# Optimization experiments

Measured on AMD Instinct MI355X. Metric: run time of the kernel, lower is better.

Reference implementation:

```python
import jax, jax.numpy as jnp
import numpy as np

H = 16        # head_nums
DN = 128      # qk_nope_head_dim
DR = 64       # qk_rope_head_dim
DV = 128      # v_head_dim
QLR = 1536    # q_lora_rank
KVLR = 512    # kv_lora_rank
HID = 2048    # hidden_dim
THETA = 10000.0
EPS = 1e-6


def _rms(x, w):
    return x * jax.lax.rsqrt(jnp.mean(x * x, axis=-1, keepdims=True) + EPS) * w


def _reorder(x):
    # replicates view(b,h,s,d//2,2).transpose(4,3).reshape: [x0,x2,...,x1,x3,...]
    return jnp.concatenate([x[..., 0::2], x[..., 1::2]], axis=-1)


def _rotate_half(x):
    h = x.shape[-1] // 2
    return jnp.concatenate([-x[..., h:], x[..., :h]], axis=-1)


def setup_inputs() -> dict:
    key = jax.random.key(0)
    ks = jax.random.split(key, 7)
    B, S = 1, 2048

    def w(k, i, o):
        return jax.random.normal(k, (i, o), jnp.float32) * (i ** -0.5)

    return {
        "x": jax.random.normal(ks[0], (B, S, HID), jnp.float32),
        "Wq_down": w(ks[1], HID, QLR),
        "q_norm_w": jnp.ones((QLR,), jnp.float32),
        "Wq_up": w(ks[2], QLR, H * (DN + DR)),
        "Wkv_down": w(ks[3], HID, KVLR + DR),
        "kv_norm_w": jnp.ones((KVLR,), jnp.float32),
        "Wkv_up": w(ks[4], KVLR, H * (DN + DV)),
        "Wo": w(ks[5], HID, HID),
        "position": jnp.broadcast_to(jnp.arange(S, dtype=jnp.int32)[None], (B, S)),
        "mask": jnp.tril(jnp.ones((S, S), bool))[None, None],  # causal [1,1,S,S]
    }


def reference(x, Wq_down, q_norm_w, Wq_up, Wkv_down, kv_norm_w, Wkv_up, Wo, position, mask):
    B, S, _ = x.shape
    # low-rank Q path: down-proj -> RMSNorm -> up-proj -> [B,H,S,DN+DR]
    q = _rms(x @ Wq_down, q_norm_w) @ Wq_up
    q = q.reshape(B, S, H, DN + DR).transpose(0, 2, 1, 3)
    q_nope, q_rope = q[..., :DN], q[..., DN:]
    # latent KV path
    ckv = x @ Wkv_down
    c, k_rope = ckv[..., :KVLR], ckv[..., KVLR:]
    c = _rms(c, kv_norm_w)
    kv = (c @ Wkv_up).reshape(B, S, H, DN + DV).transpose(0, 2, 1, 3)
    k_nope, v = kv[..., :DN], kv[..., DN:]
    k_rope = k_rope[:, None]  # [B,1,S,DR] shared across heads
    # rotary tables
    inv_freq = 1.0 / (THETA ** (jnp.arange(0, DR, 2, dtype=jnp.float32) / DR))
    t = jnp.arange(S, dtype=jnp.float32)
    emb = jnp.concatenate([jnp.outer(t, inv_freq)] * 2, axis=-1)  # [S,DR]
    cos = jnp.cos(emb)[position][:, None]  # [B,1,S,DR]
    sin = jnp.sin(emb)[position][:, None]
    qr, kr = _reorder(q_rope), _reorder(k_rope)
    q_rot = qr * cos + _rotate_half(qr) * sin
    k_rot = kr * cos + _rotate_half(kr) * sin
    q_state = jnp.concatenate([q_nope, q_rot], axis=-1)              # [B,H,S,DN+DR]
    k_state = jnp.concatenate(
        [k_nope, jnp.broadcast_to(k_rot, (B, H, S, DR))], axis=-1)   # [B,H,S,DN+DR]
    scores = jnp.einsum('bhsd,bhtd->bhst', q_state, k_state) / np.float32(np.sqrt(DV))
    scores = jnp.where(mask, scores, -jnp.inf)
    att = jax.nn.softmax(scores, axis=-1)
    out = jnp.einsum('bhst,bhtd->bhsd', att, v)
    out = out.transpose(0, 2, 1, 3).reshape(B, S, H * DV)
    return out @ Wo
```

## Files before the change

### kernel.cpp

```cpp
#include <hip/hip_runtime.h>
#include <hip/hip_bf16.h>
#include <cstddef>

#define H 16
#define DN 128
#define DR 64
#define DV 128
#define QLR 1536
#define KVLR 512
#define HID 2048
#define SLEN 2048
#define EPS 1e-6f
#define SCALE 0.08838834764831845f
#define QK_SCALE (0.08838834764831845f * 1.4426950408889634f)

typedef __attribute__((ext_vector_type(8))) short short8;
typedef __attribute__((ext_vector_type(4))) float f32x4;
typedef unsigned short u16;

__device__ __forceinline__ u16 f2bf(float f) {
    __hip_bfloat16 h = __float2bfloat16(f);
    return __builtin_bit_cast(u16, h);
}
__device__ __forceinline__ float b2f(u16 v) {
    return __bfloat162float(__builtin_bit_cast(__hip_bfloat16, v));
}
__device__ __forceinline__ unsigned pack2(float a, float b) {
    return (unsigned)f2bf(a) | ((unsigned)f2bf(b) << 16);
}

__global__ __launch_bounds__(256) void prep_all(
    const float* __restrict__ x, u16* __restrict__ xb,
    const float* __restrict__ Wqd, const float* __restrict__ Wkvd,
    const float* __restrict__ Wqu, const float* __restrict__ Wkvu,
    const float* __restrict__ Wo,
    u16* __restrict__ BtF, u16* __restrict__ Wqu_t,
    u16* __restrict__ Wkvu_t, u16* __restrict__ Wo_t)
{
    const int tid = threadIdx.x;
    if (blockIdx.x < 2048) {
        size_t base = ((size_t)blockIdx.x * 256 + tid) * 8;
        float4 v0 = *reinterpret_cast<const float4*>(x + base);
        float4 v1 = *reinterpret_cast<const float4*>(x + base + 4);
        union { short8 s; unsigned u[4]; } p;
        p.u[0] = pack2(v0.x, v0.y); p.u[1] = pack2(v0.z, v0.w);
        p.u[2] = pack2(v1.x, v1.y); p.u[3] = pack2(v1.z, v1.w);
        *reinterpret_cast<short8*>(xb + base) = p.s;
        return;
    }
    int b = blockIdx.x - 2048;
    const float* W; u16* Wt; int K, N, nx; float scale = 1.0f;
    if (b < 768)       { W = Wqd;  Wt = BtF;                          K = 2048; N = 1536; nx = 24; }
    else if (b < 1088) { b -= 768;  W = Wkvd; Wt = BtF + (size_t)1536 * 2048; K = 2048; N = 576;  nx = 10; }
    else if (b < 2240) { b -= 1088; W = Wqu;  Wt = Wqu_t;             K = 1536; N = 3072; nx = 48; scale = QK_SCALE; }
    else if (b < 2752) { b -= 2240; W = Wkvu; Wt = Wkvu_t;            K = 512;  N = 4096; nx = 64; }
    else               { b -= 2752; W = Wo;   Wt = Wo_t;              K = 2048; N = 2048; nx = 32; }
    const int bx = b % nx, by = b / nx;

    __shared__ float T[64][65];
    const int n0 = bx * 64, k0 = by * 64;
    const bool inb = (n0 < N);
    {
        int r = tid >> 4, c4 = (tid & 15) * 4;
        #pragma unroll
        for (int rr = 0; rr < 4; ++rr) {
            int row = rr * 16 + r;
            float4 v = inb ? *reinterpret_cast<const float4*>(W + (size_t)(k0 + row) * N + n0 + c4)
                           : make_float4(0.f, 0.f, 0.f, 0.f);
            T[row][c4] = v.x * scale; T[row][c4 + 1] = v.y * scale;
            T[row][c4 + 2] = v.z * scale; T[row][c4 + 3] = v.w * scale;
        }
    }
    __syncthreads();
    {
        int n = tid >> 2, kq = (tid & 3) * 16;
        unsigned u[8];
        #pragma unroll
        for (int jj = 0; jj < 8; ++jj)
            u[jj] = pack2(T[kq + 2 * jj][n], T[kq + 2 * jj + 1][n]);
        u16* dst = Wt + (size_t)(n0 + n) * K + k0 + kq;
        *reinterpret_cast<uint4*>(dst)     = make_uint4(u[0], u[1], u[2], u[3]);
        *reinterpret_cast<uint4*>(dst + 8) = make_uint4(u[4], u[5], u[6], u[7]);
    }
}

__device__ __forceinline__ void stage4(const char* Gb, const unsigned* srcOff,
                                       const int* ldsBase, u16* smemBuf, unsigned koff)
{
    #pragma unroll
    for (int j = 0; j < 4; ++j)
        __builtin_amdgcn_global_load_lds(
            (const __attribute__((address_space(1))) unsigned int*)(Gb + srcOff[j] + koff),
            (__attribute__((address_space(3))) unsigned int*)(smemBuf + ldsBase[j]),
            16, 0, 0);
}

template<bool BF16OUT>
__global__ __launch_bounds__(256) void gemm_bf16(
    const u16* __restrict__ A, const u16* __restrict__ Bt,
    void* __restrict__ Cv, int M, int N, int K)
{
    __shared__ u16 smem[2][8192];
    const int tid = threadIdx.x, lane = tid & 63, w = tid >> 6;

    const int nbx = gridDim.x, nby = gridDim.y;
    const int nwg = nbx * nby;
    int orig = blockIdx.y * nbx + blockIdx.x;
    int xcd = orig & 7, o8 = orig >> 3;
    int qq = nwg >> 3, rr = nwg & 7;
    int v = (xcd < rr ? xcd * (qq + 1) : rr * (qq + 1) + (xcd - rr) * qq) + o8;
    int bx = v / nby, by = v - bx * nby;
    const int m0 = by * 128, n0 = bx * 128;
    const size_t Kb = (size_t)K * 2;

    unsigned srcOff[4];
    int ldsBase[4];
    #pragma unroll
    for (int j = 0; j < 4; ++j) {
        int c = w * 4 + j;
        int o = (c & 7) * 1024 + lane * 16;
        int u = o ^ (((o >> 7) & 3) << 4);
        int row = u >> 6, kbyte = u & 63;
        srcOff[j] = (unsigned)((size_t)((c < 8 ? m0 : n0) + row) * Kb + kbyte);
        ldsBase[j] = (c < 8) ? (c * 512) : (4096 + (c - 8) * 512);
    }
    const char* Gb = (w < 2) ? (const char*)A : (const char*)Bt;

    const int wr = (w >> 1) * 64, wc = (w & 1) * 64;
    int aoff[4], boff[4];
    #pragma unroll
    for (int i = 0; i < 4; ++i) {
        int oa = (wr + i * 16 + (lane & 15)) * 64 + (lane >> 4) * 16;
        aoff[i] = oa ^ (((oa >> 7) & 3) << 4);
        int ob = (wc + i * 16 + (lane & 15)) * 64 + (lane >> 4) * 16;
        boff[i] = (ob ^ (((ob >> 7) & 3) << 4)) + 8192;
    }

    f32x4 acc[4][4];
    #pragma unroll
    for (int i = 0; i < 4; ++i)
        #pragma unroll
        for (int j = 0; j < 4; ++j) acc[i][j] = (f32x4){0.f, 0.f, 0.f, 0.f};

    const int NT = K >> 5;
    stage4(Gb, srcOff, ldsBase, &smem[0][0], 0);
    __syncthreads();
    int cur = 0;
    for (int t = 0; t < NT; ++t) {
        if (t + 1 < NT) stage4(Gb, srcOff, ldsBase, &smem[cur ^ 1][0], (unsigned)(t + 1) * 64);
        const char* base = (const char*)&smem[cur][0];
        short8 af[4], bfr[4];
        #pragma unroll
        for (int i = 0; i < 4; ++i) af[i] = *reinterpret_cast<const short8*>(base + aoff[i]);
        #pragma unroll
        for (int i = 0; i < 4; ++i) bfr[i] = *reinterpret_cast<const short8*>(base + boff[i]);
        __builtin_amdgcn_s_setprio(1);
        #pragma unroll
        for (int i = 0; i < 4; ++i)
            #pragma unroll
            for (int j = 0; j < 4; ++j)
                acc[i][j] = __builtin_amdgcn_mfma_f32_16x16x32_bf16(af[i], bfr[j], acc[i][j], 0, 0, 0);
        __builtin_amdgcn_s_setprio(0);
        __syncthreads();
        cur ^= 1;
    }

    #pragma unroll
    for (int i = 0; i < 4; ++i) {
        int grow0 = m0 + wr + i * 16 + ((lane >> 4) * 4);
        #pragma unroll
        for (int j = 0; j < 4; ++j) {
            int gcol = n0 + wc + j * 16 + (lane & 15);
            if (gcol < N) {
                #pragma unroll
                for (int r = 0; r < 4; ++r) {
                    float v2 = acc[i][j][r];
                    if (BF16OUT) ((u16*)Cv)[(size_t)(grow0 + r) * N + gcol] = f2bf(v2);
                    else         ((float*)Cv)[(size_t)(grow0 + r) * N + gcol] = v2;
                }
            }
        }
    }
}

__global__ __launch_bounds__(256) void rmsnorm2_bf16(
    const float* __restrict__ fC, const float* __restrict__ qw,
    const float* __restrict__ kvw, u16* __restrict__ qdb, u16* __restrict__ ckvb)
{
    const int row = blockIdx.x, tid = threadIdx.x;
    const float* p = fC + (size_t)row * 2112;
    float ssq = 0.f, ssk = 0.f;
    for (int i = tid * 4; i < 1536; i += 1024) {
        float4 v = *reinterpret_cast<const float4*>(p + i);
        ssq += v.x * v.x + v.y * v.y + v.z * v.z + v.w * v.w;
    }
    if (tid < 128) {
        float4 v = *reinterpret_cast<const float4*>(p + 1536 + tid * 4);
        ssk = v.x * v.x + v.y * v.y + v.z * v.z + v.w * v.w;
    }
    __shared__ float wsq[4], wsk[4];
    int lane = tid & 63, wv = tid >> 6;
    #pragma unroll
    for (int off = 32; off; off >>= 1) {
        ssq += __shfl_down(ssq, off);
        ssk += __shfl_down(ssk, off);
    }
    if (lane == 0) { wsq[wv] = ssq; wsk[wv] = ssk; }
    __syncthreads();
    if (tid == 0) {
        wsq[0] = rsqrtf((wsq[0] + wsq[1] + wsq[2] + wsq[3]) / 1536.f + EPS);
        wsk[0] = rsqrtf((wsk[0] + wsk[1] + wsk[2] + wsk[3]) / 512.f + EPS);
    }
    __syncthreads();
    float scq = wsq[0], sck = wsk[0];
    for (int i = tid * 4; i < 1536; i += 1024) {
        float4 v = *reinterpret_cast<const float4*>(p + i);
        float4 g = *reinterpret_cast<const float4*>(qw + i);
        *reinterpret_cast<uint2*>(qdb + (size_t)row * 1536 + i) =
            make_uint2(pack2(v.x * scq * g.x, v.y * scq * g.y),
                       pack2(v.z * scq * g.z, v.w * scq * g.w));
    }
    if (tid < 128) {
        int i = tid * 4;
        float4 v = *reinterpret_cast<const float4*>(p + 1536 + i);
        float4 g = *reinterpret_cast<const float4*>(kvw + i);
        *reinterpret_cast<uint2*>(ckvb + (size_t)row * 512 + i) =
            make_uint2(pack2(v.x * sck * g.x, v.y * sck * g.y),
                       pack2(v.z * sck * g.z, v.w * sck * g.w));
    }
}

__global__ __launch_bounds__(256) void rope_bf16(
    u16* __restrict__ q, const float* __restrict__ krsrc, int krStride,
    u16* __restrict__ krot)
{
    const int s = blockIdx.x, tid = threadIdx.x;
    __shared__ float cs[32], sn[32];
    if (tid < 32) {
        float inv = powf(10000.0f, -(float)tid / 32.0f);
        float ang = (float)s * inv;
        cs[tid] = cosf(ang); sn[tid] = sinf(ang);
    }
    __syncthreads();
    float ev[2], ov[2]; int hh[2], ii[2];
    #pragma unroll
    for (int it = 0; it < 2; ++it) {
        int pidx = tid + it * 256;
        int h = pidx >> 5, i = pidx & 31;
        hh[it] = h; ii[it] = i;
        const u16* base = q + (size_t)s * 3072 + h * 192 + 128;
        ev[it] = b2f(base[2 * i]); ov[it] = b2f(base[2 * i + 1]);
    }
    __syncthreads();
    #pragma unroll
    for (int it = 0; it < 2; ++it) {
        int h = hh[it], i = ii[it];
        u16* base = q + (size_t)s * 3072 + h * 192 + 128;
        base[i]      = f2bf(ev[it] * cs[i] - ov[it] * sn[i]);
        base[32 + i] = f2bf(ov[it] * cs[i] + ev[it] * sn[i]);
    }
    if (tid < 32) {
        int i = tid;
        float e = krsrc[(size_t)s * krStride + 2 * i];
        float o = krsrc[(size_t)s * krStride + 2 * i + 1];
        krot[(size_t)s * 64 + i]      = f2bf(e * cs[i] - o * sn[i]);
        krot[(size_t)s * 64 + 32 + i] = f2bf(o * cs[i] + e * sn[i]);
    }
}

__global__ __launch_bounds__(256, 2) void attn_chunk(
    const u16* __restrict__ qbf,
    const u16* __restrict__ kvbf,
    const u16* __restrict__ krot,
    u16* __restrict__ outb,
    u16* __restrict__ partAcc,
    float* __restrict__ partML)
{
    const int bid = blockIdx.x;
    const int xcd = bid & 7, slot = bid >> 3;
    const int h = xcd + 8 * (slot & 1);
    const int r80 = 79 - (slot >> 1);
    int qb, ch, S, poff;
    if (r80 < 8)       { qb = r80;                 ch = 0;      S = 1; poff = 0; }
    else if (r80 < 24) { int u = r80 - 8;  qb = 8 + (u >> 1);  ch = u & 1; S = 2; poff = (qb - 8) * 2 + ch; }
    else if (r80 < 48) { int u = r80 - 24; qb = 16 + u / 3;    ch = u % 3; S = 3; poff = 16 + (qb - 16) * 3 + ch; }
    else               { int u = r80 - 48; qb = 24 + (u >> 2); ch = u & 3; S = 4; poff = 40 + (qb - 24) * 4 + ch; }
    const int s0 = qb * 64;
    const int t0 = ch * 8;
    const int t1 = (t0 + 8 < qb + 1) ? (t0 + 8) : (qb + 1);
    const int slotId = h * 72 + poff;
    const int tid = threadIdx.x, lane = tid & 63, w = tid >> 6;
    const int colk = lane & 15, grp = lane >> 4, g8 = grp * 8;

    __shared__ u16 Ks[64 * 192];
    __shared__ u16 Vt[128 * 64];

    const int qg = s0 + w * 16 + colk;

    short8 qreg[6];
    {
        const u16* qp = qbf + ((size_t)qg * H + h) * 192;
        #pragma unroll
        for (int ks = 0; ks < 6; ++ks)
            qreg[ks] = *reinterpret_cast<const short8*>(qp + ks * 32 + g8);
    }

    int kt[6], kslot[6];
    #pragma unroll
    for (int it = 0; it < 6; ++it) {
        int c = it * 256 + tid;
        kt[it] = c / 24; kslot[it] = c % 24;
    }
    int vd2[2], vt8[2];
    #pragma unroll
    for (int it = 0; it < 2; ++it) {
        int c = it * 256 + tid;
        vd2[it] = c & 63; vt8[it] = c >> 6;
    }

    short8 kreg[6];
    unsigned vreg[2][8];

    auto issue_loads = [&](int t) {
        #pragma unroll
        for (int it = 0; it < 6; ++it) {
            int gk = t * 64 + kt[it];
            const u16* src = (kslot[it] < 16)
                ? kvbf + ((size_t)gk * H + h) * 256 + kslot[it] * 8
                : krot + (size_t)gk * 64 + (kslot[it] - 16) * 8;
            kreg[it] = *reinterpret_cast<const short8*>(src);
        }
        #pragma unroll
        for (int it = 0; it < 2; ++it)
            #pragma unroll
            for (int j = 0; j < 8; ++j)
                vreg[it][j] = *reinterpret_cast<const unsigned*>(
                    kvbf + ((size_t)(t * 64 + vt8[it] * 8 + j) * H + h) * 256 + 128 + 2 * vd2[it]);
    };
    auto write_lds = [&]() {
        #pragma unroll
        for (int it = 0; it < 6; ++it) {
            int sl = (kslot[it] & 24) | ((kslot[it] ^ kt[it]) & 7);
            *reinterpret_cast<short8*>(&Ks[kt[it] * 192 + sl * 8]) = kreg[it];
        }
        #pragma unroll
        for (int it = 0; it < 2; ++it) {
            uint4 lo, hi;
            unsigned* lp = &lo.x; unsigned* hp = &hi.x;
            #pragma unroll
            for (int p2 = 0; p2 < 4; ++p2) {
                unsigned a = vreg[it][2 * p2], b = vreg[it][2 * p2 + 1];
                lp[p2] = (a & 0xffffu) | (b << 16);
                hp[p2] = (a >> 16) | (b & 0xffff0000u);
            }
            int sl = (vt8[it] ^ vd2[it]) & 7;
            *reinterpret_cast<uint4*>(&Vt[vd2[it] * 64 + sl * 8]) = lo;
            *reinterpret_cast<uint4*>(&Vt[(64 + vd2[it]) * 64 + sl * 8]) = hi;
        }
    };

    float m_run = -1e30f, l_run = 0.f;
    f32x4 acc_o[8];
    #pragma unroll
    for (int i = 0; i < 8; ++i) acc_o[i] = (f32x4){0.f, 0.f, 0.f, 0.f};

    const int srcA = colk + ((grp & 1) << 5);
    const int srcB = srcA + 16;
    const bool hiSel = (grp >> 1) != 0;

    issue_loads(t0);
    for (int t = t0; t < t1; ++t) {
        __syncthreads();
        write_lds();
        __syncthreads();
        if (t + 1 < t1) issue_loads(t + 1);

        f32x4 sacc[4];
        #pragma unroll
        for (int ct = 0; ct < 4; ++ct) sacc[ct] = (f32x4){0.f, 0.f, 0.f, 0.f};
        __builtin_amdgcn_s_setprio(1);
        #pragma unroll
        for (int ks = 0; ks < 6; ++ks) {
            #pragma unroll
            for (int ct = 0; ct < 4; ++ct) {
                int key = ct * 16 + colk;
                int slotIdx = ks * 4 + grp;
                int sl = (slotIdx & 24) | ((slotIdx ^ key) & 7);
                short8 kf = *reinterpret_cast<const short8*>(&Ks[key * 192 + sl * 8]);
                sacc[ct] = __builtin_amdgcn_mfma_f32_16x16x32_bf16(kf, qreg[ks], sacc[ct], 0, 0, 0);
            }
        }
        __builtin_amdgcn_s_setprio(0);

        if (t == qb) {
            #pragma unroll
            for (int ct = 0; ct < 4; ++ct) {
                int keyb = t * 64 + ct * 16 + 4 * grp;
                #pragma unroll
                for (int r = 0; r < 4; ++r)
                    if (keyb + r > qg) sacc[ct][r] = -1e30f;
            }
        }

        float lmax = fmaxf(fmaxf(fmaxf(sacc[0][0], sacc[0][1]), fmaxf(sacc[0][2], sacc[0][3])),
                           fmaxf(fmaxf(sacc[1][0], sacc[1][1]), fmaxf(sacc[1][2], sacc[1][3])));
        lmax = fmaxf(lmax,
               fmaxf(fmaxf(fmaxf(sacc[2][0], sacc[2][1]), fmaxf(sacc[2][2], sacc[2][3])),
                     fmaxf(fmaxf(sacc[3][0], sacc[3][1]), fmaxf(sacc[3][2], sacc[3][3]))));
        bool need = lmax > m_run + 11.5f;
        if (__any((int)need)) {
            float mx = fmaxf(m_run, lmax);
            mx = fmaxf(mx, __shfl_xor(mx, 16));
            mx = fmaxf(mx, __shfl_xor(mx, 32));
            float f = exp2f(m_run - mx);
            m_run = mx;
            l_run *= f;
            #pragma unroll
            for (int i = 0; i < 8; ++i) {
                acc_o[i][0] *= f; acc_o[i][1] *= f;
                acc_o[i][2] *= f; acc_o[i][3] *= f;
            }
        }

        unsigned pku[8];
        float psum = 0.f;
        #pragma unroll
        for (int ct = 0; ct < 4; ++ct) {
            float p0 = exp2f(sacc[ct][0] - m_run);
            float p1 = exp2f(sacc[ct][1] - m_run);
            float p2 = exp2f(sacc[ct][2] - m_run);
            float p3 = exp2f(sacc[ct][3] - m_run);
            psum += (p0 + p1) + (p2 + p3);
            pku[ct * 2]     = pack2(p0, p1);
            pku[ct * 2 + 1] = pack2(p2, p3);
        }
        l_run += psum;

        __builtin_amdgcn_s_setprio(1);
        #pragma unroll
        for (int ks2 = 0; ks2 < 2; ++ks2) {
            unsigned a0 = __shfl(pku[4 * ks2 + 0], srcA);
            unsigned a1 = __shfl(pku[4 * ks2 + 1], srcA);
            unsigned a2 = __shfl(pku[4 * ks2 + 0], srcB);
            unsigned a3 = __shfl(pku[4 * ks2 + 1], srcB);
            unsigned b0 = __shfl(pku[4 * ks2 + 2], srcA);
            unsigned b1 = __shfl(pku[4 * ks2 + 3], srcA);
            unsigned b2 = __shfl(pku[4 * ks2 + 2], srcB);
            unsigned b3 = __shfl(pku[4 * ks2 + 3], srcB);
            union { short8 s; unsigned u[4]; } bq;
            bq.u[0] = hiSel ? b0 : a0;
            bq.u[1] = hiSel ? b1 : a1;
            bq.u[2] = hiSel ? b2 : a2;
            bq.u[3] = hiSel ? b3 : a3;
            #pragma unroll
            for (int ct = 0; ct < 8; ++ct) {
                int cc = ct * 16 + colk;
                int phys = (cc >> 1) + (cc & 1) * 64;
                int vsl = ((ks2 * 4 + grp) ^ phys) & 7;
                short8 vb = *reinterpret_cast<const short8*>(&Vt[phys * 64 + vsl * 8]);
                acc_o[ct] = __builtin_amdgcn_mfma_f32_16x16x32_bf16(vb, bq.s, acc_o[ct], 0, 0, 0);
            }
        }
        __builtin_amdgcn_s_setprio(0);
    }

    float l = l_run;
    l += __shfl_xor(l, 16);
    l += __shfl_xor(l, 32);
    const int rloc = w * 16 + colk;
    if (S == 1) {
        float invl = 1.0f / l;
        u16* orow = outb + (size_t)qg * 2048 + h * 128 + 4 * grp;
        #pragma unroll
        for (int ct = 0; ct < 8; ++ct) {
            uint2 pk;
            pk.x = pack2(acc_o[ct][0] * invl, acc_o[ct][1] * invl);
            pk.y = pack2(acc_o[ct][2] * invl, acc_o[ct][3] * invl);
            *reinterpret_cast<uint2*>(orow + ct * 16) = pk;
        }
    } else {
        if (grp == 0) {
            partML[(size_t)slotId * 128 + rloc * 2]     = m_run;
            partML[(size_t)slotId * 128 + rloc * 2 + 1] = l;
        }
        u16* pa = partAcc + (size_t)slotId * 8192 + rloc * 128 + 4 * grp;
        #pragma unroll
        for (int ct = 0; ct < 8; ++ct) {
            uint2 pk;
            pk.x = pack2(acc_o[ct][0], acc_o[ct][1]);
            pk.y = pack2(acc_o[ct][2], acc_o[ct][3]);
            *reinterpret_cast<uint2*>(pa + ct * 16) = pk;
        }
    }
}

__global__ __launch_bounds__(256) void attn_combine(
    const u16* __restrict__ partAcc, const float* __restrict__ partML,
    u16* __restrict__ outb)
{
    const int bid = blockIdx.x;
    const int xcd = bid & 7, s2 = bid >> 3;
    const int h = xcd + 8 * (s2 / 24);
    const int qb = 8 + s2 % 24;
    int S, poff;
    if (qb < 16)      { S = 2; poff = (qb - 8) * 2; }
    else if (qb < 24) { S = 3; poff = 16 + (qb - 16) * 3; }
    else              { S = 4; poff = 40 + (qb - 24) * 4; }
    const int base = h * 72 + poff;
    const int tid = threadIdx.x;
    const int row = tid >> 2, seg = (tid & 3) * 32;

    float mv[4], lv[4];
    float m_g = -1e30f;
    #pragma unroll
    for (int s = 0; s < 4; ++s) {
        bool ok = (s < S);
        mv[s] = ok ? partML[(size_t)(base + s) * 128 + row * 2]     : -1e30f;
        lv[s] = ok ? partML[(size_t)(base + s) * 128 + row * 2 + 1] : 0.f;
        m_g = fmaxf(m_g, mv[s]);
    }
    float l_g = 0.f, wq[4];
    #pragma unroll
    for (int s = 0; s < 4; ++s) { wq[s] = exp2f(mv[s] - m_g); l_g += wq[s] * lv[s]; }
    float inv = 1.f / l_g;
    u16* orow = outb + (size_t)(qb * 64 + row) * 2048 + h * 128 + seg;
    #pragma unroll
    for (int i = 0; i < 8; ++i) {
        float o[4] = {0.f, 0.f, 0.f, 0.f};
        #pragma unroll
        for (int s = 0; s < 4; ++s) {
            if (s < S) {
                ushort4 a = *reinterpret_cast<const ushort4*>(
                    partAcc + (size_t)(base + s) * 8192 + row * 128 + seg + i * 4);
                o[0] += wq[s] * b2f(a.x); o[1] += wq[s] * b2f(a.y);
                o[2] += wq[s] * b2f(a.z); o[3] += wq[s] * b2f(a.w);
            }
        }
        uint2 pk;
        pk.x = pack2(o[0] * inv, o[1] * inv);
        pk.y = pack2(o[2] * inv, o[3] * inv);
        *reinterpret_cast<uint2*>(orow + i * 4) = pk;
    }
}

extern "C" void kernel_launch(void* const* d_in, const int* in_sizes, int n_in,
                              void* d_out, int out_size, void* d_ws, size_t ws_size,
                              hipStream_t stream)
{
    (void)in_sizes; (void)n_in; (void)out_size; (void)ws_size;
    const float* x         = (const float*)d_in[0];
    const float* Wq_down   = (const float*)d_in[1];
    const float* q_norm_w  = (const float*)d_in[2];
    const float* Wq_up     = (const float*)d_in[3];
    const float* Wkv_down  = (const float*)d_in[4];
    const float* kv_norm_w = (const float*)d_in[5];
    const float* Wkv_up    = (const float*)d_in[6];
    const float* Wo        = (const float*)d_in[7];
    float* out = (float*)d_out;

    char* p = (char*)d_ws;
    u16* BtF     = (u16*)p;   p += (size_t)2176 * 2048 * 2;
    u16* Wkvu_t  = (u16*)p;   p += (size_t)4096 * 512  * 2;
    u16* Wo_t    = (u16*)p;   p += (size_t)2048 * 2048 * 2;
    u16* qbuf    = (u16*)p;   p += (size_t)2048 * 3072 * 2;
    u16* ckvb    = (u16*)p;   p += (size_t)2048 * 512  * 2;
    u16* kvbf    = (u16*)p;   p += (size_t)2048 * 4096 * 2;
    u16* krotb   = (u16*)p;   p += (size_t)2048 * 64   * 2;
    u16* xb      = (u16*)p;   p += (size_t)2048 * 2048 * 2;
    u16* Wqu_t   = (u16*)p;   p += (size_t)3072 * 1536 * 2;
    float* fC    = (float*)p; p += (size_t)2048 * 2112 * 4;
    u16* qdb     = (u16*)p;   p += (size_t)2048 * 1536 * 2;
    u16* attb    = (u16*)BtF;
    u16* partAcc = xb;
    float* partML  = (float*)(partAcc + (size_t)1152 * 8192);

    dim3 blk(256);
    prep_all<<<5824, blk, 0, stream>>>(x, xb, Wq_down, Wkv_down, Wq_up, Wkv_up, Wo,
                                       BtF, Wqu_t, Wkvu_t, Wo_t);

    gemm_bf16<false><<<dim3(17, 16), blk, 0, stream>>>(xb, BtF, fC, 2048, 2112, 2048);
    rmsnorm2_bf16<<<2048, blk, 0, stream>>>(fC, q_norm_w, kv_norm_w, qdb, ckvb);
    gemm_bf16<true><<<dim3(24, 16), blk, 0, stream>>>(qdb, Wqu_t, qbuf, 2048, 3072, 1536);
    gemm_bf16<true><<<dim3(32, 16), blk, 0, stream>>>(ckvb, Wkvu_t, kvbf, 2048, 4096, 512);
    rope_bf16<<<2048, blk, 0, stream>>>(qbuf, fC + 2048, 2112, krotb);

    attn_chunk<<<dim3(1280), blk, 0, stream>>>(qbuf, kvbf, krotb, attb, partAcc, partML);
    attn_combine<<<dim3(384), blk, 0, stream>>>(partAcc, partML, attb);

    gemm_bf16<false><<<dim3(16, 16), blk, 0, stream>>>(attb, Wo_t, out, 2048, 2048, 2048);
}
```

Baseline: 217.3 us.

## Pre-transpose V into a separate buffer and merge Q/KV up-projection GEMMs

Adds a vtrans kernel that writes V transposed per head ([h][d][s]) so the attention kernel loads V with 16-byte vector loads and stores it straight into LDS, replacing scattered 4-byte loads and register repacking. The Q and KV up-projection GEMMs are merged into one launch (gemm_dual) over a shared tile grid to cut launch overhead and tail idling. This adds an extra kernel pass over V (read and write about 8 MB) and a new workspace region placed at a fixed offset inside the pooled scratch area.

```diff
diff --git a/kernel.cpp b/kernel.cpp
--- a/kernel.cpp
+++ b/kernel.cpp
@@ -96,21 +96,11 @@
 }
 
 template<bool BF16OUT>
-__global__ __launch_bounds__(256) void gemm_bf16(
-    const u16* __restrict__ A, const u16* __restrict__ Bt,
-    void* __restrict__ Cv, int M, int N, int K)
-{
-    __shared__ u16 smem[2][8192];
+__device__ __forceinline__ void gemm_core(
+    const u16* __restrict__ A, const u16* __restrict__ Bt, void* __restrict__ Cv,
+    int N, int K, int m0, int n0, u16 (*smem)[8192])
+{
     const int tid = threadIdx.x, lane = tid & 63, w = tid >> 6;
-
-    const int nbx = gridDim.x, nby = gridDim.y;
-    const int nwg = nbx * nby;
-    int orig = blockIdx.y * nbx + blockIdx.x;
-    int xcd = orig & 7, o8 = orig >> 3;
-    int qq = nwg >> 3, rr = nwg & 7;
-    int v = (xcd < rr ? xcd * (qq + 1) : rr * (qq + 1) + (xcd - rr) * qq) + o8;
-    int bx = v / nby, by = v - bx * nby;
-    const int m0 = by * 128, n0 = bx * 128;
     const size_t Kb = (size_t)K * 2;
 
     unsigned srcOff[4];
@@ -183,6 +173,39 @@
     }
 }
 
+template<bool BF16OUT>
+__global__ __launch_bounds__(256) void gemm_bf16(
+    const u16* __restrict__ A, const u16* __restrict__ Bt,
+    void* __restrict__ Cv, int M, int N, int K)
+{
+    __shared__ u16 smem[2][8192];
+    const int nbx = gridDim.x, nby = gridDim.y;
+    const int nwg = nbx * nby;
+    int orig = blockIdx.y * nbx + blockIdx.x;
+    int xcd = orig & 7, o8 = orig >> 3;
+    int qq = nwg >> 3, rr = nwg & 7;
+    int v = (xcd < rr ? xcd * (qq + 1) : rr * (qq + 1) + (xcd - rr) * qq) + o8;
+    int bx = v / nby, by = v - bx * nby;
+    gemm_core<BF16OUT>(A, Bt, Cv, N, K, by * 128, bx * 128, smem);
+}
+
+__global__ __launch_bounds__(256) void gemm_dual(
+    const u16* __restrict__ Aq, const u16* __restrict__ Bq, u16* __restrict__ Cq,
+    const u16* __restrict__ Ak, const u16* __restrict__ Bk, u16* __restrict__ Ck)
+{
+    __shared__ u16 smem[2][8192];
+    int b = blockIdx.x;
+    const u16 *A, *Bt; u16* C; int N, K, nbx;
+    if (b < 384) { A = Aq; Bt = Bq; C = Cq; N = 3072; K = 1536; nbx = 24; }
+    else { b -= 384; A = Ak; Bt = Bk; C = Ck; N = 4096; K = 512; nbx = 32; }
+    const int nwg = nbx * 16;
+    int xcd = b & 7, o8 = b >> 3;
+    int qq = nwg >> 3, rr = nwg & 7;
+    int v = (xcd < rr ? xcd * (qq + 1) : rr * (qq + 1) + (xcd - rr) * qq) + o8;
+    int bx = v / 16, by = v - bx * 16;
+    gemm_core<true>(A, Bt, C, N, K, by * 128, bx * 128, smem);
+}
+
 __global__ __launch_bounds__(256) void rmsnorm2_bf16(
     const float* __restrict__ fC, const float* __restrict__ qw,
     const float* __restrict__ kvw, u16* __restrict__ qdb, u16* __restrict__ ckvb)
@@ -268,10 +291,40 @@
     }
 }
 
+__global__ __launch_bounds__(256) void vtrans(
+    const u16* __restrict__ kvbf, u16* __restrict__ vtb)
+{
+    const int bid = blockIdx.x;
+    const int h = bid & 15, rem = bid >> 4;
+    const int st = rem & 31, dt = rem >> 5;
+    __shared__ u16 T[64][72];
+    const int tid = threadIdx.x;
+    #pragma unroll
+    for (int it = 0; it < 2; ++it) {
+        int c = it * 256 + tid;
+        int r = c >> 3, c8 = (c & 7) * 8;
+        short8 v = *reinterpret_cast<const short8*>(
+            kvbf + ((size_t)(st * 64 + r) * 16 + h) * 256 + 128 + dt * 64 + c8);
+        *reinterpret_cast<short8*>(&T[r][c8]) = v;
+    }
+    __syncthreads();
+    #pragma unroll
+    for (int it = 0; it < 2; ++it) {
+        int c = it * 256 + tid;
+        int d = c >> 3, s8 = (c & 7) * 8;
+        union { short8 s; u16 e[8]; } o;
+        #pragma unroll
+        for (int j = 0; j < 8; ++j) o.e[j] = T[s8 + j][d];
+        *reinterpret_cast<short8*>(
+            vtb + ((size_t)(h * 128 + dt * 64 + d)) * 2048 + st * 64 + s8) = o.s;
+    }
+}
+
 __global__ __launch_bounds__(256, 2) void attn_chunk(
     const u16* __restrict__ qbf,
     const u16* __restrict__ kvbf,
     const u16* __restrict__ krot,
+    const u16* __restrict__ vtb,
     u16* __restrict__ outb,
     u16* __restrict__ partAcc,
     float* __restrict__ partML)
@@ -311,15 +364,14 @@
         int c = it * 256 + tid;
         kt[it] = c / 24; kslot[it] = c % 24;
     }
-    int vd2[2], vt8[2];
-    #pragma unroll
-    for (int it = 0; it < 2; ++it) {
+    int vr[4], vks_[4];
+    #pragma unroll
+    for (int it = 0; it < 4; ++it) {
         int c = it * 256 + tid;
-        vd2[it] = c & 63; vt8[it] = c >> 6;
-    }
-
-    short8 kreg[6];
-    unsigned vreg[2][8];
+        vr[it] = c >> 3; vks_[it] = c & 7;
+    }
+
+    short8 kreg[6], vregV[4];
 
     auto issue_loads = [&](int t) {
         #pragma unroll
@@ -330,12 +382,11 @@
                 : krot + (size_t)gk * 64 + (kslot[it] - 16) * 8;
             kreg[it] = *reinterpret_cast<const short8*>(src);
         }
-        #pragma unroll
-        for (int it = 0; it < 2; ++it)
-            #pragma unroll
-            for (int j = 0; j < 8; ++j)
-                vreg[it][j] = *reinterpret_cast<const unsigned*>(
-                    kvbf + ((size_t)(t * 64 + vt8[it] * 8 + j) * H + h) * 256 + 128 + 2 * vd2[it]);
+        const u16* vT = vtb + (size_t)h * 128 * 2048 + t * 64;
+        #pragma unroll
+        for (int it = 0; it < 4; ++it)
+            vregV[it] = *reinterpret_cast<const short8*>(
+                vT + (size_t)vr[it] * 2048 + vks_[it] * 8);
     };
     auto write_lds = [&]() {
         #pragma unroll
@@ -344,19 +395,9 @@
             *reinterpret_cast<short8*>(&Ks[kt[it] * 192 + sl * 8]) = kreg[it];
         }
         #pragma unroll
-        for (int it = 0; it < 2; ++it) {
-            uint4 lo, hi;
-            unsigned* lp = &lo.x; unsigned* hp = &hi.x;
-            #pragma unroll
-            for (int p2 = 0; p2 < 4; ++p2) {
-                unsigned a = vreg[it][2 * p2], b = vreg[it][2 * p2 + 1];
-                lp[p2] = (a & 0xffffu) | (b << 16);
-                hp[p2] = (a >> 16) | (b & 0xffff0000u);
-            }
-            int sl = (vt8[it] ^ vd2[it]) & 7;
-            *reinterpret_cast<uint4*>(&Vt[vd2[it] * 64 + sl * 8]) = lo;
-            *reinterpret_cast<uint4*>(&Vt[(64 + vd2[it]) * 64 + sl * 8]) = hi;
-        }
+        for (int it = 0; it < 4; ++it)
+            *reinterpret_cast<short8*>(
+                &Vt[vr[it] * 64 + ((vks_[it] ^ vr[it]) & 7) * 8]) = vregV[it];
     };
 
     float m_run = -1e30f, l_run = 0.f;
@@ -455,9 +496,8 @@
             #pragma unroll
             for (int ct = 0; ct < 8; ++ct) {
                 int cc = ct * 16 + colk;
-                int phys = (cc >> 1) + (cc & 1) * 64;
-                int vsl = ((ks2 * 4 + grp) ^ phys) & 7;
-                short8 vb = *reinterpret_cast<const short8*>(&Vt[phys * 64 + vsl * 8]);
+                int vsl = ((ks2 * 4 + grp) ^ cc) & 7;
+                short8 vb = *reinterpret_cast<const short8*>(&Vt[cc * 64 + vsl * 8]);
                 acc_o[ct] = __builtin_amdgcn_mfma_f32_16x16x32_bf16(vb, bq.s, acc_o[ct], 0, 0, 0);
             }
         }
@@ -566,6 +606,7 @@
     u16* ckvb    = (u16*)p;   p += (size_t)2048 * 512  * 2;
     u16* kvbf    = (u16*)p;   p += (size_t)2048 * 4096 * 2;
     u16* krotb   = (u16*)p;   p += (size_t)2048 * 64   * 2;
+    char* pool   = p;
     u16* xb      = (u16*)p;   p += (size_t)2048 * 2048 * 2;
     u16* Wqu_t   = (u16*)p;   p += (size_t)3072 * 1536 * 2;
     float* fC    = (float*)p; p += (size_t)2048 * 2112 * 4;
@@ -573,6 +614,7 @@
     u16* attb    = (u16*)BtF;
     u16* partAcc = xb;
     float* partML  = (float*)(partAcc + (size_t)1152 * 8192);
+    u16* vtb     = (u16*)(pool + (size_t)20 * 1024 * 1024);
 
     dim3 blk(256);
     prep_all<<<5824, blk, 0, stream>>>(x, xb, Wq_down, Wkv_down, Wq_up, Wkv_up, Wo,
@@ -580,11 +622,11 @@
 
     gemm_bf16<false><<<dim3(17, 16), blk, 0, stream>>>(xb, BtF, fC, 2048, 2112, 2048);
     rmsnorm2_bf16<<<2048, blk, 0, stream>>>(fC, q_norm_w, kv_norm_w, qdb, ckvb);
-    gemm_bf16<true><<<dim3(24, 16), blk, 0, stream>>>(qdb, Wqu_t, qbuf, 2048, 3072, 1536);
-    gemm_bf16<true><<<dim3(32, 16), blk, 0, stream>>>(ckvb, Wkvu_t, kvbf, 2048, 4096, 512);
+    gemm_dual<<<dim3(896), blk, 0, stream>>>(qdb, Wqu_t, qbuf, ckvb, Wkvu_t, kvbf);
     rope_bf16<<<2048, blk, 0, stream>>>(qbuf, fC + 2048, 2112, krotb);
-
-    attn_chunk<<<dim3(1280), blk, 0, stream>>>(qbuf, kvbf, krotb, attb, partAcc, partML);
+    vtrans<<<dim3(1024), blk, 0, stream>>>(kvbf, vtb);
+
+    attn_chunk<<<dim3(1280), blk, 0, stream>>>(qbuf, kvbf, krotb, vtb, attb, partAcc, partML);
     attn_combine<<<dim3(384), blk, 0, stream>>>(partAcc, partML, attb);
 
     gemm_bf16<false><<<dim3(16, 16), blk, 0, stream>>>(attb, Wo_t, out, 2048, 2048, 2048);
```

Measured after the change: 208.3 us. -4.1%, faster.
